# Kernel optimization log

Hardware: AMD Instinct MI355X
Metric: run time of the kernel (lower is better)

Reference implementation:

```python
import jax, jax.numpy as jnp
import numpy as np

T, IN, BATCH = 512, 512, 256
HID, WID = 1024, 512


def setup_inputs() -> dict:
    key = jax.random.key(0)
    k_x, k_wh, k_bh, k_wy, k_by, k_h0 = jax.random.split(key, 6)
    s_h = 1.0 / np.sqrt(HID + IN)  # stabilise sigmoid pre-activations
    s_y = 1.0 / np.sqrt(HID)
    return {
        "xs": jax.random.normal(k_x, (T, IN, BATCH), dtype=jnp.float32),
        "W_h": jax.random.normal(k_wh, (HID, HID + IN), dtype=jnp.float32) * s_h,
        "b_h": jax.random.normal(k_bh, (HID, 1), dtype=jnp.float32) * 0.1,
        "W_y": jax.random.normal(k_wy, (WID, HID), dtype=jnp.float32) * s_y,
        "b_y": jax.random.normal(k_by, (WID, 1), dtype=jnp.float32) * 0.1,
        "h0": jax.random.normal(k_h0, (HID, 1), dtype=jnp.float32),
    }


def reference(xs, W_h, b_h, W_y, b_y, h0):
    # xs: [T, input_size, batch]; returns ys: [T, width, batch]
    batch = xs.shape[2]
    h_init = jnp.tile(h0, (1, batch))  # [HID, batch]

    def step(h, x):
        z = jnp.concatenate([h, x], axis=0)          # [HID+IN, batch]
        h_new = jax.nn.sigmoid(W_h @ z + b_h)        # [HID, batch]
        y = jax.nn.sigmoid(W_y @ h_new + b_y)        # [WID, batch]
        return h_new, y

    _, ys = jax.lax.scan(step, h_init, xs)
    return ys
```

## Files before the change

### kernel.cpp

```cpp
#include <hip/hip_runtime.h>
#include <hip/hip_bf16.h>

#define T_STEPS 512
#define INP     512
#define NB      256
#define HID     1024
#define WID     512
#define KZ      1536
#define ZSZ     (NB * KZ)

typedef short          bf16x8   __attribute__((ext_vector_type(8)));
typedef float          f32x4    __attribute__((ext_vector_type(4)));
typedef float          f32x2    __attribute__((ext_vector_type(2)));
typedef unsigned short ushort8  __attribute__((ext_vector_type(8)));
typedef unsigned short ushort2v __attribute__((ext_vector_type(2)));
typedef unsigned short ushort4v __attribute__((ext_vector_type(4)));
typedef unsigned       uint4v   __attribute__((ext_vector_type(4)));
typedef unsigned long long u64;

__device__ __forceinline__ unsigned short f2bf(float x) {
  __hip_bfloat16 h = __float2bfloat16(x);
  return __builtin_bit_cast(unsigned short, h);
}
__device__ __forceinline__ float sigm(float x) { return 1.0f / (1.0f + __expf(-x)); }

#define ZLOAD_FAST(dst, p) \
  asm volatile("global_load_dwordx4 %0, %1, off sc0" : "=v"(dst) : "v"(p))
#define ZLOAD_SLOW(dst, p) \
  asm volatile("global_load_dwordx4 %0, %1, off sc0 sc1" : "=v"(dst) : "v"(p))
#define ZWAIT() do { \
  asm volatile("s_waitcnt vmcnt(0)" ::: "memory"); \
  __builtin_amdgcn_sched_barrier(0); \
} while (0)

template <bool FAST>
__device__ __forceinline__ void zst4(unsigned short* p, ushort2v v) {
  if constexpr (FAST) *(unsigned*)p = __builtin_bit_cast(unsigned, v);
  else __hip_atomic_store((unsigned*)p, __builtin_bit_cast(unsigned, v),
                          __ATOMIC_RELAXED, __HIP_MEMORY_SCOPE_AGENT);
}
template <bool FAST>
__device__ __forceinline__ void zst8(unsigned short* p, ushort4v v) {
  if constexpr (FAST) *(u64*)p = __builtin_bit_cast(u64, v);
  else __hip_atomic_store((u64*)p, __builtin_bit_cast(u64, v),
                          __ATOMIC_RELAXED, __HIP_MEMORY_SCOPE_AGENT);
}

__device__ __forceinline__ void poll1(unsigned* p, unsigned tgt) {
  while (__hip_atomic_load(p, __ATOMIC_RELAXED, __HIP_MEMORY_SCOPE_AGENT) < tgt)
    __builtin_amdgcn_s_sleep(1);
}
__device__ __forceinline__ void pollh(unsigned* bar, unsigned ht, unsigned xt, unsigned yt) {
  uint4v v;
  for (;;) {
    asm volatile("global_load_dwordx4 %0, %1, off sc0 sc1\n\ts_waitcnt vmcnt(0)"
                 : "=v"(v) : "v"(bar) : "memory");
    if (v.x >= ht && v.y >= xt && v.z >= yt) return;
    __builtin_amdgcn_s_sleep(1);
  }
}
__device__ __forceinline__ void arrive(unsigned* ctr) {
  asm volatile("s_waitcnt vmcnt(0)" ::: "memory");
  __syncthreads();
  if (threadIdx.x == 0)
    __hip_atomic_fetch_add(ctr, 1u, __ATOMIC_RELAXED, __HIP_MEMORY_SCOPE_AGENT);
}

__global__ void elman_setup(const float* __restrict__ h0, const float* __restrict__ xs,
                            unsigned short* __restrict__ zT, unsigned* __restrict__ bars) {
  const int b = blockIdx.x;
  if (b == 0) {
    for (int j = threadIdx.x; j < 1024; j += blockDim.x) bars[j] = 0u;
  }
  for (int k = threadIdx.x; k < KZ; k += blockDim.x) {
    const float v = (k < HID) ? h0[k] : xs[(size_t)(k - HID) * NB + b];
    zT[(size_t)b * KZ + k] = f2bf(v);
  }
  for (int i = threadIdx.x; i < INP; i += blockDim.x)
    zT[(size_t)ZSZ + (size_t)b * KZ + HID + i] = f2bf(xs[(size_t)(INP + i) * NB + b]);
}

#define PSTR 36
#define PWSZ (32 * PSTR)

template <bool FAST>
__device__ __forceinline__ void run_phases(
    const float* __restrict__ xs,
    const float* __restrict__ Wh, const float* __restrict__ bh,
    const float* __restrict__ Wy, const float* __restrict__ by,
    unsigned short* __restrict__ zT, float* __restrict__ out,
    unsigned* bar, float* P, int wg, int tid) {
  const int w = tid >> 6, lane = tid & 63;
  const int lr = lane & 15, lk = lane >> 4;

  if (wg < 128) {
    const int m0 = (wg >> 3) * 64;
    const int n0 = (wg & 7) * 32;
    const int kw = w * 192;
    bf16x8 A[4][6];
#pragma unroll
    for (int mt = 0; mt < 4; ++mt)
#pragma unroll
      for (int kc = 0; kc < 6; ++kc) {
        const float* wp = Wh + (size_t)(m0 + mt * 16 + lr) * KZ + kw + kc * 32 + lk * 8;
        const f32x4 f0 = *(const f32x4*)wp;
        const f32x4 f1 = *(const f32x4*)(wp + 4);
        ushort8 a;
#pragma unroll
        for (int e = 0; e < 4; ++e) { a[e] = f2bf(f0[e]); a[4 + e] = f2bf(f1[e]); }
        A[mt][kc] = __builtin_bit_cast(bf16x8, a);
      }
    const int lcol = tid >> 4;
    const int r2 = (tid & 15) * 2;
    f32x2 bias[2];
#pragma unroll
    for (int hf = 0; hf < 2; ++hf) bias[hf] = *(const f32x2*)&bh[m0 + hf * 32 + r2];
    float* Pw = P + w * PWSZ;

    for (int t = 0; t <= T_STEPS; ++t) {
      if (t < T_STEPS) {
        const unsigned short* zc = zT + (size_t)(t & 3) * ZSZ;
        unsigned short* zn = zT + (size_t)((t + 1) & 3) * ZSZ;
        if (t >= 1) {
          if (tid == 0) pollh(bar, 16u * (unsigned)t, 8u * (unsigned)(t - 1),
                              (t >= 2) ? 8u * (unsigned)(t - 2) : 0u);
          __syncthreads();
        }
        const unsigned short* zb = zc + (size_t)(n0 + lr) * KZ + kw + lk * 8;
        bf16x8 bfr[6][2];
#pragma unroll
        for (int kc = 0; kc < 6; ++kc)
#pragma unroll
          for (int nt = 0; nt < 2; ++nt) {
            if constexpr (FAST) ZLOAD_FAST(bfr[kc][nt], zb + nt * (16 * KZ) + kc * 32);
            else                ZLOAD_SLOW(bfr[kc][nt], zb + nt * (16 * KZ) + kc * 32);
          }
        ZWAIT();
        f32x4 acc[4][2];
#pragma unroll
        for (int mt = 0; mt < 4; ++mt)
#pragma unroll
          for (int nt = 0; nt < 2; ++nt) acc[mt][nt] = (f32x4){0.f, 0.f, 0.f, 0.f};
#pragma unroll
        for (int kc = 0; kc < 6; ++kc)
#pragma unroll
          for (int nt = 0; nt < 2; ++nt)
#pragma unroll
            for (int mt = 0; mt < 4; ++mt)
              acc[mt][nt] = __builtin_amdgcn_mfma_f32_16x16x32_bf16(A[mt][kc], bfr[kc][nt], acc[mt][nt], 0, 0, 0);
        __syncthreads();
#pragma unroll
        for (int hf = 0; hf < 2; ++hf) {
#pragma unroll
          for (int mp = 0; mp < 2; ++mp) {
            const int mt = hf * 2 + mp;
#pragma unroll
            for (int nt = 0; nt < 2; ++nt)
              *(f32x4*)&Pw[(nt * 16 + lr) * PSTR + mp * 16 + lk * 4] = acc[mt][nt];
          }
          __syncthreads();
          f32x2 s = {0.f, 0.f};
#pragma unroll
          for (int ww = 0; ww < 8; ++ww)
            s += *(const f32x2*)&P[ww * PWSZ + lcol * PSTR + r2];
          s += bias[hf];
          ushort2v o2;
          o2[0] = f2bf(sigm(s[0]));
          o2[1] = f2bf(sigm(s[1]));
          zst4<FAST>(zn + (size_t)(n0 + lcol) * KZ + m0 + hf * 32 + r2, o2);
          if (hf == 0) __syncthreads();
        }
      }
      arrive(bar + 0);
    }

  } else if (wg < 192) {
    const int idx = wg - 128;
    const int m0 = (idx >> 3) * 64;
    const int n0 = (idx & 7) * 32;
    const int kw = w * 128;
    bf16x8 A[4][4];
#pragma unroll
    for (int mt = 0; mt < 4; ++mt)
#pragma unroll
      for (int kc = 0; kc < 4; ++kc) {
        const float* wp = Wy + (size_t)(m0 + mt * 16 + lr) * HID + kw + kc * 32 + lk * 8;
        const f32x4 f0 = *(const f32x4*)wp;
        const f32x4 f1 = *(const f32x4*)(wp + 4);
        ushort8 a;
#pragma unroll
        for (int e = 0; e < 4; ++e) { a[e] = f2bf(f0[e]); a[4 + e] = f2bf(f1[e]); }
        A[mt][kc] = __builtin_bit_cast(bf16x8, a);
      }
    const int lcol = tid & 31;
    const int r2 = (tid >> 5) * 2;
    f32x2 bias[2];
#pragma unroll
    for (int hf = 0; hf < 2; ++hf) bias[hf] = *(const f32x2*)&by[m0 + hf * 32 + r2];
    float* Pw = P + w * PWSZ;

    for (int t = 0; t <= T_STEPS; ++t) {
      if (t >= 1) {
        const unsigned short* zc = zT + (size_t)(t & 3) * ZSZ;
        if (tid == 0) poll1(bar + 0, 16u * (unsigned)t);
        __syncthreads();
        const unsigned short* zb = zc + (size_t)(n0 + lr) * KZ + kw + lk * 8;
        bf16x8 bfr[4][2];
#pragma unroll
        for (int kc = 0; kc < 4; ++kc)
#pragma unroll
          for (int nt = 0; nt < 2; ++nt) {
            if constexpr (FAST) ZLOAD_FAST(bfr[kc][nt], zb + nt * (16 * KZ) + kc * 32);
            else                ZLOAD_SLOW(bfr[kc][nt], zb + nt * (16 * KZ) + kc * 32);
          }
        ZWAIT();
        f32x4 acc[4][2];
#pragma unroll
        for (int mt = 0; mt < 4; ++mt)
#pragma unroll
          for (int nt = 0; nt < 2; ++nt) acc[mt][nt] = (f32x4){0.f, 0.f, 0.f, 0.f};
#pragma unroll
        for (int kc = 0; kc < 4; ++kc)
#pragma unroll
          for (int nt = 0; nt < 2; ++nt)
#pragma unroll
            for (int mt = 0; mt < 4; ++mt)
              acc[mt][nt] = __builtin_amdgcn_mfma_f32_16x16x32_bf16(A[mt][kc], bfr[kc][nt], acc[mt][nt], 0, 0, 0);
        float* op = out + (size_t)(t - 1) * (WID * NB);
        __syncthreads();
#pragma unroll
        for (int hf = 0; hf < 2; ++hf) {
#pragma unroll
          for (int mp = 0; mp < 2; ++mp) {
            const int mt = hf * 2 + mp;
#pragma unroll
            for (int nt = 0; nt < 2; ++nt)
              *(f32x4*)&Pw[(nt * 16 + lr) * PSTR + mp * 16 + lk * 4] = acc[mt][nt];
          }
          __syncthreads();
          f32x2 s = {0.f, 0.f};
#pragma unroll
          for (int ww = 0; ww < 8; ++ww)
            s += *(const f32x2*)&P[ww * PWSZ + lcol * PSTR + r2];
          s += bias[hf];
          const int row = m0 + hf * 32 + r2;
          op[(size_t)(row + 0) * NB + n0 + lcol] = sigm(s[0]);
          op[(size_t)(row + 1) * NB + n0 + lcol] = sigm(s[1]);
          if (hf == 0) __syncthreads();
        }
      }
      arrive(bar + 2);
    }

  } else {
    const int xi = wg - 192;
    const int i0 = (xi >> 3) * 64;
    const int b0 = (xi & 7) * 32;
    const int c = tid & 31, rb = tid >> 5;
    for (int t = 0; t <= T_STEPS; ++t) {
      if (t <= T_STEPS - 3) {
        unsigned short* zx = zT + (size_t)((t + 2) & 3) * ZSZ;
        const float* xp = xs + (size_t)(t + 2) * (INP * NB) + (size_t)(i0 + rb * 4) * NB + b0 + c;
        ushort4v o;
#pragma unroll
        for (int j = 0; j < 4; ++j) o[j] = f2bf(xp[(size_t)j * NB]);
        if (t >= 2) {
          if (tid == 0) poll1(bar + 0, 16u * (unsigned)(t - 1));
        }
        __syncthreads();
        zst8<FAST>(zx + (size_t)(b0 + c) * KZ + HID + i0 + rb * 4, o);
      }
      arrive(bar + 1);
    }
  }
}

__global__ void __launch_bounds__(512, 2) elman_seq(
    const float* __restrict__ xs,
    const float* __restrict__ Wh, const float* __restrict__ bh,
    const float* __restrict__ Wy, const float* __restrict__ by,
    unsigned short* __restrict__ zT, float* __restrict__ out,
    unsigned* __restrict__ bars) {
  __shared__ float P[8 * PWSZ];
  __shared__ unsigned modeSh;
  const int wg = blockIdx.x, tid = threadIdx.x;
  unsigned* bar  = bars + (wg & 7) * 64;
  unsigned* xcds = bars + 512;
  unsigned* hbar = bars + 768;

  unsigned xcc;
  asm volatile("s_getreg_b32 %0, hwreg(HW_REG_XCC_ID)" : "=s"(xcc));
  if (tid == 0) {
    __hip_atomic_store(&xcds[wg], xcc + 1u, __ATOMIC_RELAXED, __HIP_MEMORY_SCOPE_AGENT);
    asm volatile("s_waitcnt vmcnt(0)" ::: "memory");
    __hip_atomic_fetch_add(hbar, 1u, __ATOMIC_RELAXED, __HIP_MEMORY_SCOPE_AGENT);
    while (__hip_atomic_load(hbar, __ATOMIC_RELAXED, __HIP_MEMORY_SCOPE_AGENT) < 256u)
      __builtin_amdgcn_s_sleep(1);
    const unsigned v0 = __hip_atomic_load(&xcds[wg & 7], __ATOMIC_RELAXED, __HIP_MEMORY_SCOPE_AGENT);
    unsigned m = 1u;
    for (int j = 1; j < 32; ++j)
      m &= (__hip_atomic_load(&xcds[(wg & 7) + 8 * j], __ATOMIC_RELAXED,
                              __HIP_MEMORY_SCOPE_AGENT) == v0) ? 1u : 0u;
    modeSh = m;
  }
  __syncthreads();

  if (modeSh)
    run_phases<true >(xs, Wh, bh, Wy, by, zT, out, bar, P, wg, tid);
  else
    run_phases<false>(xs, Wh, bh, Wy, by, zT, out, bar, P, wg, tid);
}

extern "C" void kernel_launch(void* const* d_in, const int* in_sizes, int n_in,
                              void* d_out, int out_size, void* d_ws, size_t ws_size,
                              hipStream_t stream) {
  (void)in_sizes; (void)n_in; (void)out_size; (void)ws_size;
  const float* xs  = (const float*)d_in[0];
  const float* W_h = (const float*)d_in[1];
  const float* b_h = (const float*)d_in[2];
  const float* W_y = (const float*)d_in[3];
  const float* b_y = (const float*)d_in[4];
  const float* h0  = (const float*)d_in[5];
  float* out = (float*)d_out;

  unsigned short* zT = (unsigned short*)d_ws;
  unsigned* bars = (unsigned*)(zT + 4 * (size_t)ZSZ);

  elman_setup<<<dim3(NB), dim3(256), 0, stream>>>(h0, xs, zT, bars);

  void* args[8];
  args[0] = (void*)&xs;  args[1] = (void*)&W_h; args[2] = (void*)&b_h;
  args[3] = (void*)&W_y; args[4] = (void*)&b_y; args[5] = (void*)&zT;
  args[6] = (void*)&out; args[7] = (void*)&bars;
  hipLaunchCooperativeKernel((void*)elman_seq, dim3(256), dim3(512), args, 0u, stream);
}
```

Measured before the change: 2.725 ms.

## Precompute input-projection MFMAs before h barrier and halve LDS reduction syncs

The recurrent workgroups now split their K range into an h part and an x part. They load the x slice of z and run its MFMAs before polling the barrier for the previous h, which takes that work off the serial critical path. The LDS partial-sum buffer is doubled so both halves of the accumulator are written at once, removing two __syncthreads per step in both the hidden and output phases. The cost is twice the shared memory and a dependency on the x-writer workgroups having stored x two steps ahead.

```diff
diff --git a/kernel.cpp b/kernel.cpp
--- a/kernel.cpp
+++ b/kernel.cpp
@@ -24,6 +24,8 @@
 }
 __device__ __forceinline__ float sigm(float x) { return 1.0f / (1.0f + __expf(-x)); }
 
+#define KEEP8(x) asm volatile("" : "+v"(x))
+
 #define ZLOAD_FAST(dst, p) \
   asm volatile("global_load_dwordx4 %0, %1, off sc0" : "=v"(dst) : "v"(p))
 #define ZLOAD_SLOW(dst, p) \
@@ -89,20 +91,22 @@
     const float* __restrict__ Wh, const float* __restrict__ bh,
     const float* __restrict__ Wy, const float* __restrict__ by,
     unsigned short* __restrict__ zT, float* __restrict__ out,
-    unsigned* bar, float* P, int wg, int tid) {
+    unsigned* line, float* P, int wg, int tid) {
   const int w = tid >> 6, lane = tid & 63;
   const int lr = lane & 15, lk = lane >> 4;
 
   if (wg < 128) {
     const int m0 = (wg >> 3) * 64;
     const int n0 = (wg & 7) * 32;
-    const int kw = w * 192;
+    const int kwh = w * 128;
+    const int kwx = HID + w * 64;
     bf16x8 A[4][6];
 #pragma unroll
     for (int mt = 0; mt < 4; ++mt)
 #pragma unroll
       for (int kc = 0; kc < 6; ++kc) {
-        const float* wp = Wh + (size_t)(m0 + mt * 16 + lr) * KZ + kw + kc * 32 + lk * 8;
+        const int kg = (kc < 4) ? (kwh + kc * 32) : (kwx + (kc - 4) * 32);
+        const float* wp = Wh + (size_t)(m0 + mt * 16 + lr) * KZ + kg + lk * 8;
         const f32x4 f0 = *(const f32x4*)wp;
         const f32x4 f1 = *(const f32x4*)(wp + 4);
         ushort8 a;
@@ -115,63 +119,82 @@
     f32x2 bias[2];
 #pragma unroll
     for (int hf = 0; hf < 2; ++hf) bias[hf] = *(const f32x2*)&bh[m0 + hf * 32 + r2];
-    float* Pw = P + w * PWSZ;
+    float* Pw = P + w * (2 * PWSZ);
 
     for (int t = 0; t <= T_STEPS; ++t) {
+#pragma unroll
+      for (int mt = 0; mt < 4; ++mt)
+#pragma unroll
+        for (int kc = 0; kc < 6; ++kc) KEEP8(A[mt][kc]);
       if (t < T_STEPS) {
         const unsigned short* zc = zT + (size_t)(t & 3) * ZSZ;
         unsigned short* zn = zT + (size_t)((t + 1) & 3) * ZSZ;
+        const unsigned short* zbh = zc + (size_t)(n0 + lr) * KZ + kwh + lk * 8;
+        const unsigned short* zbx = zc + (size_t)(n0 + lr) * KZ + kwx + lk * 8;
+        bf16x8 fx[2][2];
+#pragma unroll
+        for (int j = 0; j < 2; ++j)
+#pragma unroll
+          for (int nt = 0; nt < 2; ++nt) {
+            if constexpr (FAST) ZLOAD_FAST(fx[j][nt], zbx + nt * (16 * KZ) + j * 32);
+            else                ZLOAD_SLOW(fx[j][nt], zbx + nt * (16 * KZ) + j * 32);
+          }
+        ZWAIT();
+        f32x4 acc[4][2];
+#pragma unroll
+        for (int mt = 0; mt < 4; ++mt)
+#pragma unroll
+          for (int nt = 0; nt < 2; ++nt) acc[mt][nt] = (f32x4){0.f, 0.f, 0.f, 0.f};
+#pragma unroll
+        for (int j = 0; j < 2; ++j)
+#pragma unroll
+          for (int nt = 0; nt < 2; ++nt)
+#pragma unroll
+            for (int mt = 0; mt < 4; ++mt)
+              acc[mt][nt] = __builtin_amdgcn_mfma_f32_16x16x32_bf16(A[mt][4 + j], fx[j][nt], acc[mt][nt], 0, 0, 0);
         if (t >= 1) {
-          if (tid == 0) pollh(bar, 16u * (unsigned)t, 8u * (unsigned)(t - 1),
+          if (tid == 0) pollh(line, 16u * (unsigned)t, 8u * (unsigned)(t - 1),
                               (t >= 2) ? 8u * (unsigned)(t - 2) : 0u);
           __syncthreads();
         }
-        const unsigned short* zb = zc + (size_t)(n0 + lr) * KZ + kw + lk * 8;
-        bf16x8 bfr[6][2];
-#pragma unroll
-        for (int kc = 0; kc < 6; ++kc)
+        bf16x8 fh[4][2];
+#pragma unroll
+        for (int kc = 0; kc < 4; ++kc)
 #pragma unroll
           for (int nt = 0; nt < 2; ++nt) {
-            if constexpr (FAST) ZLOAD_FAST(bfr[kc][nt], zb + nt * (16 * KZ) + kc * 32);
-            else                ZLOAD_SLOW(bfr[kc][nt], zb + nt * (16 * KZ) + kc * 32);
+            if constexpr (FAST) ZLOAD_FAST(fh[kc][nt], zbh + nt * (16 * KZ) + kc * 32);
+            else                ZLOAD_SLOW(fh[kc][nt], zbh + nt * (16 * KZ) + kc * 32);
           }
         ZWAIT();
-        f32x4 acc[4][2];
-#pragma unroll
-        for (int mt = 0; mt < 4; ++mt)
-#pragma unroll
-          for (int nt = 0; nt < 2; ++nt) acc[mt][nt] = (f32x4){0.f, 0.f, 0.f, 0.f};
-#pragma unroll
-        for (int kc = 0; kc < 6; ++kc)
+#pragma unroll
+        for (int kc = 0; kc < 4; ++kc)
 #pragma unroll
           for (int nt = 0; nt < 2; ++nt)
 #pragma unroll
             for (int mt = 0; mt < 4; ++mt)
-              acc[mt][nt] = __builtin_amdgcn_mfma_f32_16x16x32_bf16(A[mt][kc], bfr[kc][nt], acc[mt][nt], 0, 0, 0);
+              acc[mt][nt] = __builtin_amdgcn_mfma_f32_16x16x32_bf16(A[mt][kc], fh[kc][nt], acc[mt][nt], 0, 0, 0);
+#pragma unroll
+        for (int hf = 0; hf < 2; ++hf)
+#pragma unroll
+          for (int mp = 0; mp < 2; ++mp)
+#pragma unroll
+            for (int nt = 0; nt < 2; ++nt)
+              *(f32x4*)&Pw[hf * PWSZ + (nt * 16 + lr) * PSTR + mp * 16 + lk * 4] = acc[hf * 2 + mp][nt];
         __syncthreads();
 #pragma unroll
         for (int hf = 0; hf < 2; ++hf) {
-#pragma unroll
-          for (int mp = 0; mp < 2; ++mp) {
-            const int mt = hf * 2 + mp;
-#pragma unroll
-            for (int nt = 0; nt < 2; ++nt)
-              *(f32x4*)&Pw[(nt * 16 + lr) * PSTR + mp * 16 + lk * 4] = acc[mt][nt];
-          }
-          __syncthreads();
           f32x2 s = {0.f, 0.f};
 #pragma unroll
           for (int ww = 0; ww < 8; ++ww)
-            s += *(const f32x2*)&P[ww * PWSZ + lcol * PSTR + r2];
+            s += *(const f32x2*)&P[ww * (2 * PWSZ) + hf * PWSZ + lcol * PSTR + r2];
           s += bias[hf];
           ushort2v o2;
           o2[0] = f2bf(sigm(s[0]));
           o2[1] = f2bf(sigm(s[1]));
           zst4<FAST>(zn + (size_t)(n0 + lcol) * KZ + m0 + hf * 32 + r2, o2);
-          if (hf == 0) __syncthreads();
         }
       }
-      arrive(bar + 0);
+      arrive(line + 0);
     }
 
   } else if (wg < 192) {
@@ -197,21 +220,25 @@
     f32x2 bias[2];
 #pragma unroll
     for (int hf = 0; hf < 2; ++hf) bias[hf] = *(const f32x2*)&by[m0 + hf * 32 + r2];
-    float* Pw = P + w * PWSZ;
+    float* Pw = P + w * (2 * PWSZ);
 
     for (int t = 0; t <= T_STEPS; ++t) {
+#pragma unroll
+      for (int mt = 0; mt < 4; ++mt)
+#pragma unroll
+        for (int kc = 0; kc < 4; ++kc) KEEP8(A[mt][kc]);
       if (t >= 1) {
         const unsigned short* zc = zT + (size_t)(t & 3) * ZSZ;
-        if (tid == 0) poll1(bar + 0, 16u * (unsigned)t);
+        if (tid == 0) poll1(line + 0, 16u * (unsigned)t);
         __syncthreads();
         const unsigned short* zb = zc + (size_t)(n0 + lr) * KZ + kw + lk * 8;
-        bf16x8 bfr[4][2];
+        bf16x8 fb[4][2];
 #pragma unroll
         for (int kc = 0; kc < 4; ++kc)
 #pragma unroll
           for (int nt = 0; nt < 2; ++nt) {
-            if constexpr (FAST) ZLOAD_FAST(bfr[kc][nt], zb + nt * (16 * KZ) + kc * 32);
-            else                ZLOAD_SLOW(bfr[kc][nt], zb + nt * (16 * KZ) + kc * 32);
+            if constexpr (FAST) ZLOAD_FAST(fb[kc][nt], zb + nt * (16 * KZ) + kc * 32);
+            else                ZLOAD_SLOW(fb[kc][nt], zb + nt * (16 * KZ) + kc * 32);
           }
         ZWAIT();
         f32x4 acc[4][2];
@@ -225,31 +252,29 @@
           for (int nt = 0; nt < 2; ++nt)
 #pragma unroll
             for (int mt = 0; mt < 4; ++mt)
-              acc[mt][nt] = __builtin_amdgcn_mfma_f32_16x16x32_bf16(A[mt][kc], bfr[kc][nt], acc[mt][nt], 0, 0, 0);
+              acc[mt][nt] = __builtin_amdgcn_mfma_f32_16x16x32_bf16(A[mt][kc], fb[kc][nt], acc[mt][nt], 0, 0, 0);
         float* op = out + (size_t)(t - 1) * (WID * NB);
+#pragma unroll
+        for (int hf = 0; hf < 2; ++hf)
+#pragma unroll
+          for (int mp = 0; mp < 2; ++mp)
+#pragma unroll
+            for (int nt = 0; nt < 2; ++nt)
+              *(f32x4*)&Pw[hf * PWSZ + (nt * 16 + lr) * PSTR + mp * 16 + lk * 4] = acc[hf * 2 + mp][nt];
         __syncthreads();
 #pragma unroll
         for (int hf = 0; hf < 2; ++hf) {
-#pragma unroll
-          for (int mp = 0; mp < 2; ++mp) {
-            const int mt = hf * 2 + mp;
-#pragma unroll
-            for (int nt = 0; nt < 2; ++nt)
-              *(f32x4*)&Pw[(nt * 16 + lr) * PSTR + mp * 16 + lk * 4] = acc[mt][nt];
-          }
-          __syncthreads();
           f32x2 s = {0.f, 0.f};
 #pragma unroll
           for (int ww = 0; ww < 8; ++ww)
-            s += *(const f32x2*)&P[ww * PWSZ + lcol * PSTR + r2];
+            s += *(const f32x2*)&P[ww * (2 * PWSZ) + hf * PWSZ + lcol * PSTR + r2];
           s += bias[hf];
           const int row = m0 + hf * 32 + r2;
           op[(size_t)(row + 0) * NB + n0 + lcol] = sigm(s[0]);
           op[(size_t)(row + 1) * NB + n0 + lcol] = sigm(s[1]);
-          if (hf == 0) __syncthreads();
         }
       }
-      arrive(bar + 2);
+      arrive(line + 2);
     }
 
   } else {
@@ -264,13 +289,11 @@
         ushort4v o;
 #pragma unroll
         for (int j = 0; j < 4; ++j) o[j] = f2bf(xp[(size_t)j * NB]);
-        if (t >= 2) {
-          if (tid == 0) poll1(bar + 0, 16u * (unsigned)(t - 1));
-        }
+        if (t >= 2 && tid == 0) poll1(line + 0, 16u * (unsigned)(t - 1));
         __syncthreads();
         zst8<FAST>(zx + (size_t)(b0 + c) * KZ + HID + i0 + rb * 4, o);
       }
-      arrive(bar + 1);
+      arrive(line + 1);
     }
   }
 }
@@ -281,10 +304,10 @@
     const float* __restrict__ Wy, const float* __restrict__ by,
     unsigned short* __restrict__ zT, float* __restrict__ out,
     unsigned* __restrict__ bars) {
-  __shared__ float P[8 * PWSZ];
+  __shared__ float P[16 * PWSZ];
   __shared__ unsigned modeSh;
   const int wg = blockIdx.x, tid = threadIdx.x;
-  unsigned* bar  = bars + (wg & 7) * 64;
+  unsigned* line = bars + (wg & 7) * 64;
   unsigned* xcds = bars + 512;
   unsigned* hbar = bars + 768;
 
@@ -306,9 +329,9 @@
   __syncthreads();
 
   if (modeSh)
-    run_phases<true >(xs, Wh, bh, Wy, by, zT, out, bar, P, wg, tid);
+    run_phases<true >(xs, Wh, bh, Wy, by, zT, out, line, P, wg, tid);
   else
-    run_phases<false>(xs, Wh, bh, Wy, by, zT, out, bar, P, wg, tid);
+    run_phases<false>(xs, Wh, bh, Wy, by, zT, out, line, P, wg, tid);
 }
 
 extern "C" void kernel_launch(void* const* d_in, const int* in_sizes, int n_in,
```

Measured after the change: 2.847 ms. +4.5%, slower.

## Fuse hidden, output and input-staging roles into every workgroup of a 128-block grid

Applied to the files above, without the earlier changes.

Replaces the three specialized workgroup roles (hidden GEMM, output GEMM, x staging) with a single uniform workgroup that does all three each step. The output projection runs lagged by one step and the x conversion two steps ahead. Each workgroup then waits on one counter instead of three. The grid shrinks from 256 to 128 blocks with one block per CU, which reduces barrier participants and polling overhead but puts more work and register pressure on each block's critical path.

```diff
diff --git a/kernel.cpp b/kernel.cpp
--- a/kernel.cpp
+++ b/kernel.cpp
@@ -14,8 +14,6 @@
 typedef float          f32x2    __attribute__((ext_vector_type(2)));
 typedef unsigned short ushort8  __attribute__((ext_vector_type(8)));
 typedef unsigned short ushort2v __attribute__((ext_vector_type(2)));
-typedef unsigned short ushort4v __attribute__((ext_vector_type(4)));
-typedef unsigned       uint4v   __attribute__((ext_vector_type(4)));
 typedef unsigned long long u64;
 
 __device__ __forceinline__ unsigned short f2bf(float x) {
@@ -39,25 +37,10 @@
   else __hip_atomic_store((unsigned*)p, __builtin_bit_cast(unsigned, v),
                           __ATOMIC_RELAXED, __HIP_MEMORY_SCOPE_AGENT);
 }
-template <bool FAST>
-__device__ __forceinline__ void zst8(unsigned short* p, ushort4v v) {
-  if constexpr (FAST) *(u64*)p = __builtin_bit_cast(u64, v);
-  else __hip_atomic_store((u64*)p, __builtin_bit_cast(u64, v),
-                          __ATOMIC_RELAXED, __HIP_MEMORY_SCOPE_AGENT);
-}
 
 __device__ __forceinline__ void poll1(unsigned* p, unsigned tgt) {
   while (__hip_atomic_load(p, __ATOMIC_RELAXED, __HIP_MEMORY_SCOPE_AGENT) < tgt)
     __builtin_amdgcn_s_sleep(1);
-}
-__device__ __forceinline__ void pollh(unsigned* bar, unsigned ht, unsigned xt, unsigned yt) {
-  uint4v v;
-  for (;;) {
-    asm volatile("global_load_dwordx4 %0, %1, off sc0 sc1\n\ts_waitcnt vmcnt(0)"
-                 : "=v"(v) : "v"(bar) : "memory");
-    if (v.x >= ht && v.y >= xt && v.z >= yt) return;
-    __builtin_amdgcn_s_sleep(1);
-  }
 }
 __device__ __forceinline__ void arrive(unsigned* ctr) {
   asm volatile("s_waitcnt vmcnt(0)" ::: "memory");
@@ -89,202 +72,171 @@
     const float* __restrict__ Wh, const float* __restrict__ bh,
     const float* __restrict__ Wy, const float* __restrict__ by,
     unsigned short* __restrict__ zT, float* __restrict__ out,
-    unsigned* bar, float* P, int wg, int tid) {
+    unsigned* line, float* P, int wg, int tid) {
   const int w = tid >> 6, lane = tid & 63;
   const int lr = lane & 15, lk = lane >> 4;
-
-  if (wg < 128) {
-    const int m0 = (wg >> 3) * 64;
-    const int n0 = (wg & 7) * 32;
-    const int kw = w * 192;
-    bf16x8 A[4][6];
-#pragma unroll
-    for (int mt = 0; mt < 4; ++mt)
-#pragma unroll
-      for (int kc = 0; kc < 6; ++kc) {
-        const float* wp = Wh + (size_t)(m0 + mt * 16 + lr) * KZ + kw + kc * 32 + lk * 8;
-        const f32x4 f0 = *(const f32x4*)wp;
-        const f32x4 f1 = *(const f32x4*)(wp + 4);
-        ushort8 a;
-#pragma unroll
-        for (int e = 0; e < 4; ++e) { a[e] = f2bf(f0[e]); a[4 + e] = f2bf(f1[e]); }
-        A[mt][kc] = __builtin_bit_cast(bf16x8, a);
-      }
-    const int lcol = tid >> 4;
-    const int r2 = (tid & 15) * 2;
-    f32x2 bias[2];
-#pragma unroll
-    for (int hf = 0; hf < 2; ++hf) bias[hf] = *(const f32x2*)&bh[m0 + hf * 32 + r2];
-    float* Pw = P + w * PWSZ;
-
-    for (int t = 0; t <= T_STEPS; ++t) {
-      if (t < T_STEPS) {
-        const unsigned short* zc = zT + (size_t)(t & 3) * ZSZ;
-        unsigned short* zn = zT + (size_t)((t + 1) & 3) * ZSZ;
-        if (t >= 1) {
-          if (tid == 0) pollh(bar, 16u * (unsigned)t, 8u * (unsigned)(t - 1),
-                              (t >= 2) ? 8u * (unsigned)(t - 2) : 0u);
-          __syncthreads();
+  const int m0h = (wg >> 3) * 64;
+  const int m0y = (wg >> 3) * 32;
+  const int i0x = (wg >> 3) * 32;
+  const int n0  = (wg & 7) * 32;
+  const int kwh = w * 192;
+  const int kwy = w * 128;
+
+  bf16x8 Ah[4][6];
+#pragma unroll
+  for (int mt = 0; mt < 4; ++mt)
+#pragma unroll
+    for (int kc = 0; kc < 6; ++kc) {
+      const float* wp = Wh + (size_t)(m0h + mt * 16 + lr) * KZ + kwh + kc * 32 + lk * 8;
+      const f32x4 f0 = *(const f32x4*)wp;
+      const f32x4 f1 = *(const f32x4*)(wp + 4);
+      ushort8 a;
+#pragma unroll
+      for (int e = 0; e < 4; ++e) { a[e] = f2bf(f0[e]); a[4 + e] = f2bf(f1[e]); }
+      Ah[mt][kc] = __builtin_bit_cast(bf16x8, a);
+    }
+  bf16x8 Ay[2][4];
+#pragma unroll
+  for (int mt = 0; mt < 2; ++mt)
+#pragma unroll
+    for (int kc = 0; kc < 4; ++kc) {
+      const float* wp = Wy + (size_t)(m0y + mt * 16 + lr) * HID + kwy + kc * 32 + lk * 8;
+      const f32x4 f0 = *(const f32x4*)wp;
+      const f32x4 f1 = *(const f32x4*)(wp + 4);
+      ushort8 a;
+#pragma unroll
+      for (int e = 0; e < 4; ++e) { a[e] = f2bf(f0[e]); a[4 + e] = f2bf(f1[e]); }
+      Ay[mt][kc] = __builtin_bit_cast(bf16x8, a);
+    }
+
+  const int lcolh = tid >> 4, r2h = (tid & 15) * 2;
+  const int lcoly = tid & 31, r2y = (tid >> 5) * 2;
+  const int cx = tid & 31,  rx = (tid >> 5) * 2;
+  f32x2 biasH[2];
+#pragma unroll
+  for (int hf = 0; hf < 2; ++hf) biasH[hf] = *(const f32x2*)&bh[m0h + hf * 32 + r2h];
+  const f32x2 biasY = *(const f32x2*)&by[m0y + r2y];
+  float* Ph = P;
+  float* Py = P + 8 * PWSZ;
+  float* PwH = Ph + w * PWSZ;
+  float* PwY = Py + w * PWSZ;
+
+  for (int t = 0; t <= T_STEPS + 1; ++t) {
+    float xv0 = 0.f, xv1 = 0.f;
+    if (t <= T_STEPS - 3) {
+      const float* xp = xs + (size_t)(t + 2) * (INP * NB) + (size_t)(i0x + rx) * NB + n0 + cx;
+      xv0 = xp[0];
+      xv1 = xp[NB];
+    }
+    if (t >= 2) {
+      const unsigned short* zb = zT + (size_t)((t - 1) & 3) * ZSZ + (size_t)(n0 + lr) * KZ + kwy + lk * 8;
+      bf16x8 fb[4][2];
+#pragma unroll
+      for (int kc = 0; kc < 4; ++kc)
+#pragma unroll
+        for (int nt = 0; nt < 2; ++nt) {
+          if constexpr (FAST) ZLOAD_FAST(fb[kc][nt], zb + nt * (16 * KZ) + kc * 32);
+          else                ZLOAD_SLOW(fb[kc][nt], zb + nt * (16 * KZ) + kc * 32);
         }
-        const unsigned short* zb = zc + (size_t)(n0 + lr) * KZ + kw + lk * 8;
-        bf16x8 bfr[6][2];
-#pragma unroll
-        for (int kc = 0; kc < 6; ++kc)
-#pragma unroll
-          for (int nt = 0; nt < 2; ++nt) {
-            if constexpr (FAST) ZLOAD_FAST(bfr[kc][nt], zb + nt * (16 * KZ) + kc * 32);
-            else                ZLOAD_SLOW(bfr[kc][nt], zb + nt * (16 * KZ) + kc * 32);
-          }
-        ZWAIT();
-        f32x4 acc[4][2];
-#pragma unroll
-        for (int mt = 0; mt < 4; ++mt)
-#pragma unroll
-          for (int nt = 0; nt < 2; ++nt) acc[mt][nt] = (f32x4){0.f, 0.f, 0.f, 0.f};
-#pragma unroll
-        for (int kc = 0; kc < 6; ++kc)
+      ZWAIT();
+      f32x4 ay[2][2];
+#pragma unroll
+      for (int mt = 0; mt < 2; ++mt)
+#pragma unroll
+        for (int nt = 0; nt < 2; ++nt) ay[mt][nt] = (f32x4){0.f, 0.f, 0.f, 0.f};
+#pragma unroll
+      for (int kc = 0; kc < 4; ++kc)
+#pragma unroll
+        for (int nt = 0; nt < 2; ++nt)
+#pragma unroll
+          for (int mt = 0; mt < 2; ++mt)
+            ay[mt][nt] = __builtin_amdgcn_mfma_f32_16x16x32_bf16(Ay[mt][kc], fb[kc][nt], ay[mt][nt], 0, 0, 0);
+#pragma unroll
+      for (int mt = 0; mt < 2; ++mt)
+#pragma unroll
+        for (int nt = 0; nt < 2; ++nt)
+          *(f32x4*)&PwY[(nt * 16 + lr) * PSTR + mt * 16 + lk * 4] = ay[mt][nt];
+      __syncthreads();
+      f32x2 s = {0.f, 0.f};
+#pragma unroll
+      for (int ww = 0; ww < 8; ++ww)
+        s += *(const f32x2*)&Py[ww * PWSZ + lcoly * PSTR + r2y];
+      s += biasY;
+      float* op = out + (size_t)(t - 2) * (WID * NB);
+      op[(size_t)(m0y + r2y + 0) * NB + n0 + lcoly] = sigm(s[0]);
+      op[(size_t)(m0y + r2y + 1) * NB + n0 + lcoly] = sigm(s[1]);
+    }
+    if (t <= T_STEPS - 3) {
+      ushort2v o;
+      o[0] = f2bf(xv0);
+      o[1] = f2bf(xv1);
+      zst4<FAST>(zT + (size_t)((t + 2) & 3) * ZSZ + (size_t)(n0 + cx) * KZ + HID + i0x + rx, o);
+    }
+    if (t >= 1 && t <= T_STEPS) {
+      if (tid == 0) poll1(line, 16u * (unsigned)t);
+      __syncthreads();
+    }
+    if (t < T_STEPS) {
+      const unsigned short* zc = zT + (size_t)(t & 3) * ZSZ;
+      unsigned short* zn = zT + (size_t)((t + 1) & 3) * ZSZ;
+      const unsigned short* zb = zc + (size_t)(n0 + lr) * KZ + kwh + lk * 8;
+      bf16x8 bfr[6][2];
+#pragma unroll
+      for (int kc = 0; kc < 6; ++kc)
+#pragma unroll
+        for (int nt = 0; nt < 2; ++nt) {
+          if constexpr (FAST) ZLOAD_FAST(bfr[kc][nt], zb + nt * (16 * KZ) + kc * 32);
+          else                ZLOAD_SLOW(bfr[kc][nt], zb + nt * (16 * KZ) + kc * 32);
+        }
+      ZWAIT();
+      f32x4 acc[4][2];
+#pragma unroll
+      for (int mt = 0; mt < 4; ++mt)
+#pragma unroll
+        for (int nt = 0; nt < 2; ++nt) acc[mt][nt] = (f32x4){0.f, 0.f, 0.f, 0.f};
+#pragma unroll
+      for (int kc = 0; kc < 6; ++kc)
+#pragma unroll
+        for (int nt = 0; nt < 2; ++nt)
+#pragma unroll
+          for (int mt = 0; mt < 4; ++mt)
+            acc[mt][nt] = __builtin_amdgcn_mfma_f32_16x16x32_bf16(Ah[mt][kc], bfr[kc][nt], acc[mt][nt], 0, 0, 0);
+#pragma unroll
+      for (int hf = 0; hf < 2; ++hf) {
+#pragma unroll
+        for (int mp = 0; mp < 2; ++mp) {
+          const int mt = hf * 2 + mp;
 #pragma unroll
           for (int nt = 0; nt < 2; ++nt)
-#pragma unroll
-            for (int mt = 0; mt < 4; ++mt)
-              acc[mt][nt] = __builtin_amdgcn_mfma_f32_16x16x32_bf16(A[mt][kc], bfr[kc][nt], acc[mt][nt], 0, 0, 0);
-        __syncthreads();
-#pragma unroll
-        for (int hf = 0; hf < 2; ++hf) {
-#pragma unroll
-          for (int mp = 0; mp < 2; ++mp) {
-            const int mt = hf * 2 + mp;
-#pragma unroll
-            for (int nt = 0; nt < 2; ++nt)
-              *(f32x4*)&Pw[(nt * 16 + lr) * PSTR + mp * 16 + lk * 4] = acc[mt][nt];
-          }
-          __syncthreads();
-          f32x2 s = {0.f, 0.f};
-#pragma unroll
-          for (int ww = 0; ww < 8; ++ww)
-            s += *(const f32x2*)&P[ww * PWSZ + lcol * PSTR + r2];
-          s += bias[hf];
-          ushort2v o2;
-          o2[0] = f2bf(sigm(s[0]));
-          o2[1] = f2bf(sigm(s[1]));
-          zst4<FAST>(zn + (size_t)(n0 + lcol) * KZ + m0 + hf * 32 + r2, o2);
-          if (hf == 0) __syncthreads();
-        }
-      }
-      arrive(bar + 0);
-    }
-
-  } else if (wg < 192) {
-    const int idx = wg - 128;
-    const int m0 = (idx >> 3) * 64;
-    const int n0 = (idx & 7) * 32;
-    const int kw = w * 128;
-    bf16x8 A[4][4];
-#pragma unroll
-    for (int mt = 0; mt < 4; ++mt)
-#pragma unroll
-      for (int kc = 0; kc < 4; ++kc) {
-        const float* wp = Wy + (size_t)(m0 + mt * 16 + lr) * HID + kw + kc * 32 + lk * 8;
-        const f32x4 f0 = *(const f32x4*)wp;
-        const f32x4 f1 = *(const f32x4*)(wp + 4);
-        ushort8 a;
-#pragma unroll
-        for (int e = 0; e < 4; ++e) { a[e] = f2bf(f0[e]); a[4 + e] = f2bf(f1[e]); }
-        A[mt][kc] = __builtin_bit_cast(bf16x8, a);
-      }
-    const int lcol = tid & 31;
-    const int r2 = (tid >> 5) * 2;
-    f32x2 bias[2];
-#pragma unroll
-    for (int hf = 0; hf < 2; ++hf) bias[hf] = *(const f32x2*)&by[m0 + hf * 32 + r2];
-    float* Pw = P + w * PWSZ;
-
-    for (int t = 0; t <= T_STEPS; ++t) {
-      if (t >= 1) {
-        const unsigned short* zc = zT + (size_t)(t & 3) * ZSZ;
-        if (tid == 0) poll1(bar + 0, 16u * (unsigned)t);
-        __syncthreads();
-        const unsigned short* zb = zc + (size_t)(n0 + lr) * KZ + kw + lk * 8;
-        bf16x8 bfr[4][2];
-#pragma unroll
-        for (int kc = 0; kc < 4; ++kc)
-#pragma unroll
-          for (int nt = 0; nt < 2; ++nt) {
-            if constexpr (FAST) ZLOAD_FAST(bfr[kc][nt], zb + nt * (16 * KZ) + kc * 32);
-            else                ZLOAD_SLOW(bfr[kc][nt], zb + nt * (16 * KZ) + kc * 32);
-          }
-        ZWAIT();
-        f32x4 acc[4][2];
-#pragma unroll
-        for (int mt = 0; mt < 4; ++mt)
-#pragma unroll
-          for (int nt = 0; nt < 2; ++nt) acc[mt][nt] = (f32x4){0.f, 0.f, 0.f, 0.f};
-#pragma unroll
-        for (int kc = 0; kc < 4; ++kc)
-#pragma unroll
-          for (int nt = 0; nt < 2; ++nt)
-#pragma unroll
-            for (int mt = 0; mt < 4; ++mt)
-              acc[mt][nt] = __builtin_amdgcn_mfma_f32_16x16x32_bf16(A[mt][kc], bfr[kc][nt], acc[mt][nt], 0, 0, 0);
-        float* op = out + (size_t)(t - 1) * (WID * NB);
-        __syncthreads();
-#pragma unroll
-        for (int hf = 0; hf < 2; ++hf) {
-#pragma unroll
-          for (int mp = 0; mp < 2; ++mp) {
-            const int mt = hf * 2 + mp;
-#pragma unroll
-            for (int nt = 0; nt < 2; ++nt)
-              *(f32x4*)&Pw[(nt * 16 + lr) * PSTR + mp * 16 + lk * 4] = acc[mt][nt];
-          }
-          __syncthreads();
-          f32x2 s = {0.f, 0.f};
-#pragma unroll
-          for (int ww = 0; ww < 8; ++ww)
-            s += *(const f32x2*)&P[ww * PWSZ + lcol * PSTR + r2];
-          s += bias[hf];
-          const int row = m0 + hf * 32 + r2;
-          op[(size_t)(row + 0) * NB + n0 + lcol] = sigm(s[0]);
-          op[(size_t)(row + 1) * NB + n0 + lcol] = sigm(s[1]);
-          if (hf == 0) __syncthreads();
-        }
-      }
-      arrive(bar + 2);
-    }
-
-  } else {
-    const int xi = wg - 192;
-    const int i0 = (xi >> 3) * 64;
-    const int b0 = (xi & 7) * 32;
-    const int c = tid & 31, rb = tid >> 5;
-    for (int t = 0; t <= T_STEPS; ++t) {
-      if (t <= T_STEPS - 3) {
-        unsigned short* zx = zT + (size_t)((t + 2) & 3) * ZSZ;
-        const float* xp = xs + (size_t)(t + 2) * (INP * NB) + (size_t)(i0 + rb * 4) * NB + b0 + c;
-        ushort4v o;
-#pragma unroll
-        for (int j = 0; j < 4; ++j) o[j] = f2bf(xp[(size_t)j * NB]);
-        if (t >= 2) {
-          if (tid == 0) poll1(bar + 0, 16u * (unsigned)(t - 1));
+            *(f32x4*)&PwH[(nt * 16 + lr) * PSTR + mp * 16 + lk * 4] = acc[mt][nt];
         }
         __syncthreads();
-        zst8<FAST>(zx + (size_t)(b0 + c) * KZ + HID + i0 + rb * 4, o);
+        f32x2 s = {0.f, 0.f};
+#pragma unroll
+        for (int ww = 0; ww < 8; ++ww)
+          s += *(const f32x2*)&Ph[ww * PWSZ + lcolh * PSTR + r2h];
+        s += biasH[hf];
+        ushort2v o2;
+        o2[0] = f2bf(sigm(s[0]));
+        o2[1] = f2bf(sigm(s[1]));
+        zst4<FAST>(zn + (size_t)(n0 + lcolh) * KZ + m0h + hf * 32 + r2h, o2);
+        if (hf == 0) __syncthreads();
       }
-      arrive(bar + 1);
-    }
-  }
-}
-
-__global__ void __launch_bounds__(512, 2) elman_seq(
+    }
+    arrive(line);
+  }
+}
+
+__global__ void __launch_bounds__(512, 1) elman_seq(
     const float* __restrict__ xs,
     const float* __restrict__ Wh, const float* __restrict__ bh,
     const float* __restrict__ Wy, const float* __restrict__ by,
     unsigned short* __restrict__ zT, float* __restrict__ out,
     unsigned* __restrict__ bars) {
-  __shared__ float P[8 * PWSZ];
+  __shared__ float P[16 * PWSZ];
   __shared__ unsigned modeSh;
   const int wg = blockIdx.x, tid = threadIdx.x;
-  unsigned* bar  = bars + (wg & 7) * 64;
+  unsigned* line = bars + (wg & 7) * 64;
   unsigned* xcds = bars + 512;
   unsigned* hbar = bars + 768;
 
@@ -294,11 +246,11 @@
     __hip_atomic_store(&xcds[wg], xcc + 1u, __ATOMIC_RELAXED, __HIP_MEMORY_SCOPE_AGENT);
     asm volatile("s_waitcnt vmcnt(0)" ::: "memory");
     __hip_atomic_fetch_add(hbar, 1u, __ATOMIC_RELAXED, __HIP_MEMORY_SCOPE_AGENT);
-    while (__hip_atomic_load(hbar, __ATOMIC_RELAXED, __HIP_MEMORY_SCOPE_AGENT) < 256u)
+    while (__hip_atomic_load(hbar, __ATOMIC_RELAXED, __HIP_MEMORY_SCOPE_AGENT) < 128u)
       __builtin_amdgcn_s_sleep(1);
     const unsigned v0 = __hip_atomic_load(&xcds[wg & 7], __ATOMIC_RELAXED, __HIP_MEMORY_SCOPE_AGENT);
     unsigned m = 1u;
-    for (int j = 1; j < 32; ++j)
+    for (int j = 1; j < 16; ++j)
       m &= (__hip_atomic_load(&xcds[(wg & 7) + 8 * j], __ATOMIC_RELAXED,
                               __HIP_MEMORY_SCOPE_AGENT) == v0) ? 1u : 0u;
     modeSh = m;
@@ -306,9 +258,9 @@
   __syncthreads();
 
   if (modeSh)
-    run_phases<true >(xs, Wh, bh, Wy, by, zT, out, bar, P, wg, tid);
+    run_phases<true >(xs, Wh, bh, Wy, by, zT, out, line, P, wg, tid);
   else
-    run_phases<false>(xs, Wh, bh, Wy, by, zT, out, bar, P, wg, tid);
+    run_phases<false>(xs, Wh, bh, Wy, by, zT, out, line, P, wg, tid);
 }
 
 extern "C" void kernel_launch(void* const* d_in, const int* in_sizes, int n_in,
@@ -332,5 +284,5 @@
   args[0] = (void*)&xs;  args[1] = (void*)&W_h; args[2] = (void*)&b_h;
   args[3] = (void*)&W_y; args[4] = (void*)&b_y; args[5] = (void*)&zT;
   args[6] = (void*)&out; args[7] = (void*)&bars;
-  hipLaunchCooperativeKernel((void*)elman_seq, dim3(256), dim3(512), args, 0u, stream);
-}
+  hipLaunchCooperativeKernel((void*)elman_seq, dim3(128), dim3(512), args, 0u, stream);
+}
```

New measurement: 3.670 ms. +34.7%, slower.
